# Optimization experiments

Measured on AMD Instinct MI355X. Metric: run time of the kernel, lower is better.

The kernel has to match this reference:

```python
import jax, jax.numpy as jnp
import numpy as np

NUM_HEADS = 32
HEAD_DIM = 128
HIDDEN = NUM_HEADS * HEAD_DIM  # 4096
GROUP = 128                    # fp8 activation group size (cols)
EPS = 1e-6
FP8_MAX = 448.0                # float8_e4m3fn max


def _fp8_roundtrip(v):
    # emulate fp8 e4m3 quantization: cast down then back up
    return v.astype(jnp.float8_e4m3fn).astype(jnp.float32)


def setup_inputs() -> dict:
    key = jax.random.key(0)
    k1, k2, k3 = jax.random.split(key, 3)
    x = jax.random.normal(k1, (8192, HIDDEN), dtype=jnp.float32)
    z = jax.random.normal(k2, (8192, HIDDEN), dtype=jnp.float32)
    norm_weight = jnp.ones((HEAD_DIM,), dtype=jnp.float32)
    w = jax.random.normal(k3, (HIDDEN, HIDDEN), dtype=jnp.float32) * (HIDDEN ** -0.5)
    return {"x": x, "z": z, "norm_weight": norm_weight, "w": w}


def reference(x, z, norm_weight, w):
    n = x.shape[0]
    # elementwise relu before the gated norm
    x = jax.nn.relu(x)
    z = jax.nn.relu(z)
    # per-head view: (N*H, D)
    xh = x.reshape(-1, HEAD_DIM)
    zh = z.reshape(-1, HEAD_DIM)
    # RMSNormGated, norm_before_gate=True: rmsnorm(x) * weight * silu(z)
    var = jnp.mean(xh * xh, axis=-1, keepdims=True)
    normed = xh * jax.lax.rsqrt(var + EPS) * norm_weight
    gated = normed * (zh * jax.nn.sigmoid(zh))  # silu gate
    merged = gated.reshape(n, HIDDEN)
    # dynamic per-group (1, GROUP) fp8 quantization of activations
    g = merged.reshape(n, HIDDEN // GROUP, GROUP)
    a_scale = jnp.maximum(jnp.max(jnp.abs(g), axis=-1, keepdims=True), 1e-12) / FP8_MAX
    a_dq = _fp8_roundtrip(g / a_scale) * a_scale
    a = a_dq.reshape(n, HIDDEN)
    # static per-block (GROUP, GROUP) fp8 quantization of the weight
    wb = w.reshape(HIDDEN // GROUP, GROUP, HIDDEN // GROUP, GROUP)
    w_scale = jnp.maximum(jnp.max(jnp.abs(wb), axis=(1, 3), keepdims=True), 1e-12) / FP8_MAX
    w_dq = (_fp8_roundtrip(wb / w_scale) * w_scale).reshape(HIDDEN, HIDDEN)
    # linear: out = a @ W^T
    return a @ w_dq.T
```

## Files before the change

kernel.cpp:

```cpp
#include <hip/hip_runtime.h>
#include <cstdint>

#define M_ROWS 8192
#define HIDDEN 4096
#define GROUP  128
#define NGRP   32
#define FP8MAX 448.0f
#define EPSV   1e-6f

using float4_t = __attribute__((ext_vector_type(4))) float;

__device__ __forceinline__ void async_ld16(const void* g, void* l) {
    __builtin_amdgcn_global_load_lds(
        (const __attribute__((address_space(1))) void*)g,
        (__attribute__((address_space(3))) void*)l, 16, 0, 0);
}

__global__ __launch_bounds__(256)
void act_quant_kernel(const float* __restrict__ x, const float* __restrict__ z,
                      const float* __restrict__ nw,
                      uint8_t* __restrict__ a, float* __restrict__ a_sc) {
    const int tid  = threadIdx.x;
    const int lane = tid & 63;
    const int wv   = tid >> 6;
    const long gh  = (long)blockIdx.x * 4 + wv;
    const long row = gh >> 5;
    const int  h   = (int)(gh & 31);
    const long base = row * HIDDEN + (long)h * GROUP + lane * 2;

    float2 xv = *(const float2*)(x + base);
    float2 zv = *(const float2*)(z + base);
    float x0 = fmaxf(xv.x, 0.f), x1 = fmaxf(xv.y, 0.f);
    float z0 = fmaxf(zv.x, 0.f), z1 = fmaxf(zv.y, 0.f);

    float ss = x0 * x0 + x1 * x1;
    #pragma unroll
    for (int o = 32; o > 0; o >>= 1) ss += __shfl_xor(ss, o, 64);
    const float rstd = 1.0f / sqrtf(ss * (1.0f / 128.0f) + EPSV);

    const float w0 = nw[lane * 2], w1 = nw[lane * 2 + 1];
    const float s0 = z0 / (1.f + expf(-z0));
    const float s1 = z1 / (1.f + expf(-z1));
    const float g0 = x0 * rstd * w0 * s0;
    const float g1 = x1 * rstd * w1 * s1;

    float am = fmaxf(fabsf(g0), fabsf(g1));
    #pragma unroll
    for (int o = 32; o > 0; o >>= 1) am = fmaxf(am, __shfl_xor(am, o, 64));
    const float scale = fmaxf(am, 1e-12f) / FP8MAX;

    const int packed = __builtin_amdgcn_cvt_pk_fp8_f32(g0 / scale, g1 / scale, 0, false);
    *(uint16_t*)(a + base) = (uint16_t)(packed & 0xffff);
    if (lane == 0) a_sc[row * NGRP + h] = scale;
}

__global__ __launch_bounds__(256)
void w_quant_kernel(const float* __restrict__ w, uint8_t* __restrict__ wq,
                    float* __restrict__ w_sc) {
    const int jb = blockIdx.x, kb = blockIdx.y;
    const int tid  = threadIdx.x;
    const int lane = tid & 63;
    const int wv   = tid >> 6;
    const int r     = tid >> 1;
    const int cbase = (tid & 1) * 64;
    const float* src = w + (long)(jb * 128 + r) * HIDDEN + kb * 128 + cbase;

    float am = 0.f;
    #pragma unroll
    for (int i = 0; i < 16; ++i) {
        float4_t v = *(const float4_t*)(src + i * 4);
        am = fmaxf(am, fmaxf(fmaxf(fabsf(v[0]), fabsf(v[1])),
                             fmaxf(fabsf(v[2]), fabsf(v[3]))));
    }
    #pragma unroll
    for (int o = 32; o > 0; o >>= 1) am = fmaxf(am, __shfl_xor(am, o, 64));

    __shared__ float red[4];
    if (lane == 0) red[wv] = am;
    __syncthreads();
    am = fmaxf(fmaxf(red[0], red[1]), fmaxf(red[2], red[3]));
    const float scale = fmaxf(am, 1e-12f) / FP8MAX;
    if (tid == 0) w_sc[jb * NGRP + kb] = scale;

    uint8_t* dst = wq + (long)(jb * 128 + r) * HIDDEN + kb * 128 + cbase;
    #pragma unroll
    for (int i = 0; i < 16; ++i) {
        float4_t v = *(const float4_t*)(src + i * 4);
        int p = __builtin_amdgcn_cvt_pk_fp8_f32(v[0] / scale, v[1] / scale, 0, false);
        p     = __builtin_amdgcn_cvt_pk_fp8_f32(v[2] / scale, v[3] / scale, p, true);
        *(uint32_t*)(dst + i * 4) = (uint32_t)p;
    }
}

__global__ __launch_bounds__(256, 2)
void gemm_fp8_scaled(const uint8_t* __restrict__ A, const float* __restrict__ As,
                     const uint8_t* __restrict__ B, const float* __restrict__ Bs,
                     float* __restrict__ C) {
    constexpr int K = HIDDEN;
    __shared__ uint8_t lA[128 * 128];
    __shared__ uint8_t lB[128 * 128];
    __shared__ float   lAs[NGRP * 128];

    const int tid  = threadIdx.x;
    const int lane = tid & 63;
    const int wv   = tid >> 6;
    const long row0 = (long)blockIdx.x * 128;
    const long col0 = (long)blockIdx.y * 128;

    for (int i = tid; i < NGRP * 128; i += 256) {
        int r = i & 127, g = i >> 7;
        lAs[g * 128 + r] = As[(row0 + r) * NGRP + g];
    }

    const int m    = lane & 15;
    const int quad = lane >> 4;
    const int wm = (wv & 1) * 64;
    const int wn = (wv >> 1) * 64;

    const int srow = tid >> 3;
    const int slot = tid & 7;

    float4_t acc[4][4] = {};

    for (int kg = 0; kg < NGRP; ++kg) {
        #pragma unroll
        for (int p = 0; p < 4; ++p) {
            int r = p * 32 + srow;
            int c = slot ^ (r & 7);
            async_ld16(A + (row0 + r) * K + kg * 128 + c * 16,
                       &lA[p * 4096 + tid * 16]);
        }
        #pragma unroll
        for (int p = 0; p < 4; ++p) {
            int r = p * 32 + srow;
            int c = slot ^ (r & 7);
            async_ld16(B + (col0 + r) * K + kg * 128 + c * 16,
                       &lB[p * 4096 + tid * 16]);
        }
        __syncthreads();

        float4_t part[4][4] = {};
        #pragma unroll
        for (int ks = 0; ks < 4; ++ks) {
            const int c16 = ks * 2 + (quad >> 1);
            const int hof = (quad & 1) * 8;
            long af[4], bf[4];
            #pragma unroll
            for (int t = 0; t < 4; ++t) {
                int r = wm + t * 16 + m;
                af[t] = *(const long*)&lA[r * 128 + ((c16 ^ (r & 7)) * 16) + hof];
            }
            #pragma unroll
            for (int t = 0; t < 4; ++t) {
                int r = wn + t * 16 + m;
                bf[t] = *(const long*)&lB[r * 128 + ((c16 ^ (r & 7)) * 16) + hof];
            }
            #pragma unroll
            for (int mt = 0; mt < 4; ++mt)
                #pragma unroll
                for (int nt = 0; nt < 4; ++nt)
                    part[mt][nt] = __builtin_amdgcn_mfma_f32_16x16x32_fp8_fp8(
                        af[mt], bf[nt], part[mt][nt], 0, 0, 0);
        }
        __syncthreads();

        const float wsc = Bs[blockIdx.y * NGRP + kg];
        #pragma unroll
        for (int mt = 0; mt < 4; ++mt) {
            float4_t as4 = *(const float4_t*)&lAs[kg * 128 + wm + mt * 16 + quad * 4];
            float s0 = as4[0] * wsc, s1 = as4[1] * wsc;
            float s2 = as4[2] * wsc, s3 = as4[3] * wsc;
            #pragma unroll
            for (int nt = 0; nt < 4; ++nt) {
                acc[mt][nt][0] += s0 * part[mt][nt][0];
                acc[mt][nt][1] += s1 * part[mt][nt][1];
                acc[mt][nt][2] += s2 * part[mt][nt][2];
                acc[mt][nt][3] += s3 * part[mt][nt][3];
            }
        }
    }

    #pragma unroll
    for (int mt = 0; mt < 4; ++mt)
        #pragma unroll
        for (int nt = 0; nt < 4; ++nt) {
            const long r  = row0 + wm + mt * 16 + quad * 4;
            const long cc = col0 + wn + nt * 16 + m;
            #pragma unroll
            for (int g = 0; g < 4; ++g)
                C[(r + g) * HIDDEN + cc] = acc[mt][nt][g];
        }
}

extern "C" void kernel_launch(void* const* d_in, const int* in_sizes, int n_in,
                              void* d_out, int out_size, void* d_ws, size_t ws_size,
                              hipStream_t stream) {
    const float* x  = (const float*)d_in[0];
    const float* z  = (const float*)d_in[1];
    const float* nw = (const float*)d_in[2];
    const float* w  = (const float*)d_in[3];
    float* out = (float*)d_out;

    uint8_t* ws8   = (uint8_t*)d_ws;
    uint8_t* a_fp8 = ws8;
    uint8_t* w_fp8 = ws8 + (size_t)M_ROWS * HIDDEN;
    float*   a_sc  = (float*)(w_fp8 + (size_t)HIDDEN * HIDDEN);
    float*   w_sc  = a_sc + (size_t)M_ROWS * NGRP;

    act_quant_kernel<<<M_ROWS * NGRP / 4, 256, 0, stream>>>(x, z, nw, a_fp8, a_sc);
    w_quant_kernel<<<dim3(NGRP, NGRP), 256, 0, stream>>>(w, w_fp8, w_sc);
    gemm_fp8_scaled<<<dim3(M_ROWS / 128, HIDDEN / 128), 256, 0, stream>>>(
        a_fp8, a_sc, w_fp8, w_sc, out);
}
```

Measured before the change: 598.6 us.

## Vectorize activation quant, transpose activation scales, prefold weight scale, raise occupancy

The activation quant kernel now has each half-wave handle one 128-column group with float4 loads and 32-bit fp8 stores, so every wave covers two groups instead of one. Activation scales are written transposed (group-major), which makes the GEMM's scale preload coalesced. The GEMM also multiplies the weight block scale into the shared scale table once, removing per-k-group multiplies from the inner loop. The GEMM launch bound is raised to 3 waves per SIMD, which may force register spills given the 64-float accumulator plus partials.

Result: slower. 746.8 us (+24.8%).

```diff
diff --git a/kernel.cpp b/kernel.cpp
--- a/kernel.cpp
+++ b/kernel.cpp
@@ -17,41 +17,50 @@
 }
 
 __global__ __launch_bounds__(256)
-void act_quant_kernel(const float* __restrict__ x, const float* __restrict__ z,
+void act_quant_kernel(const float4_t* __restrict__ x, const float4_t* __restrict__ z,
                       const float* __restrict__ nw,
-                      uint8_t* __restrict__ a, float* __restrict__ a_sc) {
+                      uint32_t* __restrict__ a, float* __restrict__ a_scT) {
     const int tid  = threadIdx.x;
     const int lane = tid & 63;
+    const int l32  = lane & 31;
+    const int sub  = lane >> 5;
     const int wv   = tid >> 6;
-    const long gh  = (long)blockIdx.x * 4 + wv;
+    const long gh  = (long)blockIdx.x * 8 + wv * 2 + sub;
     const long row = gh >> 5;
     const int  h   = (int)(gh & 31);
-    const long base = row * HIDDEN + (long)h * GROUP + lane * 2;
-
-    float2 xv = *(const float2*)(x + base);
-    float2 zv = *(const float2*)(z + base);
-    float x0 = fmaxf(xv.x, 0.f), x1 = fmaxf(xv.y, 0.f);
-    float z0 = fmaxf(zv.x, 0.f), z1 = fmaxf(zv.y, 0.f);
-
-    float ss = x0 * x0 + x1 * x1;
-    #pragma unroll
-    for (int o = 32; o > 0; o >>= 1) ss += __shfl_xor(ss, o, 64);
+    const long base4 = row * (HIDDEN / 4) + (long)h * 32 + l32;
+
+    float4_t xv = x[base4];
+    float4_t zv = z[base4];
+    float g[4];
+    float ss = 0.f;
+    #pragma unroll
+    for (int j = 0; j < 4; ++j) {
+        float xr = fmaxf(xv[j], 0.f);
+        g[j] = xr;
+        ss += xr * xr;
+    }
+    #pragma unroll
+    for (int o = 16; o > 0; o >>= 1) ss += __shfl_xor(ss, o, 64);
     const float rstd = 1.0f / sqrtf(ss * (1.0f / 128.0f) + EPSV);
 
-    const float w0 = nw[lane * 2], w1 = nw[lane * 2 + 1];
-    const float s0 = z0 / (1.f + expf(-z0));
-    const float s1 = z1 / (1.f + expf(-z1));
-    const float g0 = x0 * rstd * w0 * s0;
-    const float g1 = x1 * rstd * w1 * s1;
-
-    float am = fmaxf(fabsf(g0), fabsf(g1));
-    #pragma unroll
-    for (int o = 32; o > 0; o >>= 1) am = fmaxf(am, __shfl_xor(am, o, 64));
+    const float4_t w4 = *(const float4_t*)(nw + l32 * 4);
+    float am = 0.f;
+    #pragma unroll
+    for (int j = 0; j < 4; ++j) {
+        float zr = fmaxf(zv[j], 0.f);
+        float si = zr / (1.f + expf(-zr));
+        g[j] = g[j] * rstd * w4[j] * si;
+        am = fmaxf(am, fabsf(g[j]));
+    }
+    #pragma unroll
+    for (int o = 16; o > 0; o >>= 1) am = fmaxf(am, __shfl_xor(am, o, 64));
     const float scale = fmaxf(am, 1e-12f) / FP8MAX;
 
-    const int packed = __builtin_amdgcn_cvt_pk_fp8_f32(g0 / scale, g1 / scale, 0, false);
-    *(uint16_t*)(a + base) = (uint16_t)(packed & 0xffff);
-    if (lane == 0) a_sc[row * NGRP + h] = scale;
+    int p = __builtin_amdgcn_cvt_pk_fp8_f32(g[0] / scale, g[1] / scale, 0, false);
+    p     = __builtin_amdgcn_cvt_pk_fp8_f32(g[2] / scale, g[3] / scale, p, true);
+    a[base4] = (uint32_t)p;
+    if (l32 == 0) a_scT[(long)h * M_ROWS + row] = scale;
 }
 
 __global__ __launch_bounds__(256)
@@ -92,8 +101,8 @@
     }
 }
 
-__global__ __launch_bounds__(256, 2)
-void gemm_fp8_scaled(const uint8_t* __restrict__ A, const float* __restrict__ As,
+__global__ __launch_bounds__(256, 3)
+void gemm_fp8_scaled(const uint8_t* __restrict__ A, const float* __restrict__ AsT,
                      const uint8_t* __restrict__ B, const float* __restrict__ Bs,
                      float* __restrict__ C) {
     constexpr int K = HIDDEN;
@@ -109,7 +118,7 @@
 
     for (int i = tid; i < NGRP * 128; i += 256) {
         int r = i & 127, g = i >> 7;
-        lAs[g * 128 + r] = As[(row0 + r) * NGRP + g];
+        lAs[g * 128 + r] = AsT[(long)g * M_ROWS + row0 + r] * Bs[blockIdx.y * NGRP + g];
     }
 
     const int m    = lane & 15;
@@ -164,18 +173,15 @@
         }
         __syncthreads();
 
-        const float wsc = Bs[blockIdx.y * NGRP + kg];
         #pragma unroll
         for (int mt = 0; mt < 4; ++mt) {
-            float4_t as4 = *(const float4_t*)&lAs[kg * 128 + wm + mt * 16 + quad * 4];
-            float s0 = as4[0] * wsc, s1 = as4[1] * wsc;
-            float s2 = as4[2] * wsc, s3 = as4[3] * wsc;
+            float4_t s4 = *(const float4_t*)&lAs[kg * 128 + wm + mt * 16 + quad * 4];
             #pragma unroll
             for (int nt = 0; nt < 4; ++nt) {
-                acc[mt][nt][0] += s0 * part[mt][nt][0];
-                acc[mt][nt][1] += s1 * part[mt][nt][1];
-                acc[mt][nt][2] += s2 * part[mt][nt][2];
-                acc[mt][nt][3] += s3 * part[mt][nt][3];
+                acc[mt][nt][0] += s4[0] * part[mt][nt][0];
+                acc[mt][nt][1] += s4[1] * part[mt][nt][1];
+                acc[mt][nt][2] += s4[2] * part[mt][nt][2];
+                acc[mt][nt][3] += s4[3] * part[mt][nt][3];
             }
         }
     }
@@ -204,11 +210,12 @@
     uint8_t* ws8   = (uint8_t*)d_ws;
     uint8_t* a_fp8 = ws8;
     uint8_t* w_fp8 = ws8 + (size_t)M_ROWS * HIDDEN;
-    float*   a_sc  = (float*)(w_fp8 + (size_t)HIDDEN * HIDDEN);
-    float*   w_sc  = a_sc + (size_t)M_ROWS * NGRP;
-
-    act_quant_kernel<<<M_ROWS * NGRP / 4, 256, 0, stream>>>(x, z, nw, a_fp8, a_sc);
+    float*   a_scT = (float*)(w_fp8 + (size_t)HIDDEN * HIDDEN);
+    float*   w_sc  = a_scT + (size_t)NGRP * M_ROWS;
+
+    act_quant_kernel<<<M_ROWS * NGRP / 8, 256, 0, stream>>>(
+        (const float4_t*)x, (const float4_t*)z, nw, (uint32_t*)a_fp8, a_scT);
     w_quant_kernel<<<dim3(NGRP, NGRP), 256, 0, stream>>>(w, w_fp8, w_sc);
     gemm_fp8_scaled<<<dim3(M_ROWS / 128, HIDDEN / 128), 256, 0, stream>>>(
-        a_fp8, a_sc, w_fp8, w_sc, out);
-}
+        a_fp8, a_scT, w_fp8, w_sc, out);
+}
```
